# Performance work log

Hardware: AMD Instinct MI355X
Metric: run time of the kernel (lower is better)

The kernel has to match this reference:

```python
import jax, jax.numpy as jnp
import numpy as np

D_MODEL = 1024
N_HEADS = 16
HEAD = D_MODEL // N_HEADS
B, T = 4, 2048


def setup_inputs() -> dict:
    key = jax.random.key(0)
    ks = jax.random.split(key, 8)
    s = 0.02
    return {
        "x_enc": jax.random.normal(ks[0], (B, T, D_MODEL), dtype=jnp.float32),
        "x_dec": jax.random.normal(ks[1], (B, T, D_MODEL), dtype=jnp.float32),
        "mask": jnp.zeros((B, T, T), dtype=jnp.float32),
        "Wq": jax.random.normal(ks[2], (D_MODEL, D_MODEL), dtype=jnp.float32) * s,
        "bq": jnp.zeros((D_MODEL,), dtype=jnp.float32),
        "Wkv": jax.random.normal(ks[3], (D_MODEL, 2 * D_MODEL), dtype=jnp.float32) * s,
        "bkv": jnp.zeros((2 * D_MODEL,), dtype=jnp.float32),
        "Wo": jax.random.normal(ks[4], (D_MODEL, D_MODEL), dtype=jnp.float32) * s,
        "bo": jnp.zeros((D_MODEL,), dtype=jnp.float32),
    }


def reference(x_enc, x_dec, mask, Wq, bq, Wkv, bkv, Wo, bo):
    b, t, c = x_enc.shape
    # projections
    kv = x_enc @ Wkv + bkv                     # [B,T,2C]
    q = x_dec @ Wq + bq                        # [B,T,C]
    # split heads (replicates torch reshape of interleaved kv)
    kv = kv.reshape(b, t, N_HEADS, 2 * HEAD).transpose(0, 2, 1, 3)  # [B,H,T,2hs]
    q = q.reshape(b, t, N_HEADS, HEAD).transpose(0, 2, 1, 3)        # [B,H,T,hs]
    k, v = kv[..., :HEAD], kv[..., HEAD:]
    # attention
    scores = jnp.einsum("bhqd,bhkd->bhqk", q, k) / np.sqrt(HEAD).astype(np.float32)
    scores = scores + mask[:, None, :, :]      # additive mask, broadcast over heads
    attn = jax.nn.softmax(scores, axis=-1)
    res = jnp.einsum("bhqk,bhkd->bhqd", attn, v)   # [B,H,T,hs]
    res = res.transpose(0, 2, 1, 3).reshape(b, t, c)
    return res @ Wo + bo
```

## Files before the change

### kernel.cpp

```cpp
#include <hip/hip_runtime.h>
#include <hip/hip_bf16.h>
#include <math.h>


#define D_MODEL 1024
#define NH      16
#define HEAD    64
#define BATCH   4
#define SEQ     2048
#define QB      128

#define LOG2E   1.44269504088896f

typedef unsigned int   u32;
typedef unsigned short u16;
typedef __attribute__((ext_vector_type(8))) short s16x8;
typedef __attribute__((ext_vector_type(4))) float f32x4;

__device__ __forceinline__ u16 tobf(float f) {
    u32 u = __builtin_bit_cast(u32, f);
    return (u16)((u + 0x7fffu + ((u >> 16) & 1u)) >> 16);
}
__device__ __forceinline__ float frombf(u16 u) {
    return __builtin_bit_cast(float, (u32)u << 16);
}
__device__ __forceinline__ u32 cvtpk(float a, float b) {
    u32 r;
    asm("v_cvt_pk_bf16_f32 %0, %1, %2" : "=v"(r) : "v"(a), "v"(b));
    return r;
}

__device__ __forceinline__ void gl_lds16(const void* g, void* l) {
    __builtin_amdgcn_global_load_lds(
        (const __attribute__((address_space(1))) u32*)g,
        (__attribute__((address_space(3))) u32*)l, 16, 0, 0);
}

__global__ __launch_bounds__(256) void cast_bf16(
    const float* __restrict__ in, u16* __restrict__ out, int n)
{
    int i = (blockIdx.x * 256 + threadIdx.x) * 4;
    if (i < n) {
        float4 v = *(const float4*)(in + i);
        ushort4 o = make_ushort4(tobf(v.x), tobf(v.y), tobf(v.z), tobf(v.w));
        *(ushort4*)(out + i) = o;
    }
}

__global__ __launch_bounds__(256) void mask_prep(
    const float* __restrict__ mask, u16* __restrict__ mp)
{
    const size_t gt = (size_t)blockIdx.x * 256 + threadIdx.x;
    const int l = (int)(gt & 63);
    const size_t tile = gt >> 6;
    const int kt = (int)(tile & 127);
    const size_t bq = tile >> 7;
    const int qt = (int)(bq & 127);
    const int b  = (int)(bq >> 7);
    const int q15 = l & 15, quad = l >> 4;
    const int q = qt*16 + q15;
    const int k = kt*16 + quad*4;
    float4 v = *(const float4*)&mask[((size_t)(b*SEQ + q))*SEQ + k];
    ushort4 o = make_ushort4(tobf(v.x * LOG2E), tobf(v.y * LOG2E),
                             tobf(v.z * LOG2E), tobf(v.w * LOG2E));
    *(ushort4*)&mp[tile*256 + (size_t)l*4] = o;
}

__global__ __launch_bounds__(256) void transpose_cast(
    const float* __restrict__ W, u16* __restrict__ WT, int K, int N)
{
    __shared__ __align__(16) float tile[32][33];
    const int n0 = blockIdx.x * 32, k0 = blockIdx.y * 32;
    const int r = threadIdx.x >> 3, c4 = (threadIdx.x & 7) * 4;
    float4 v = *(const float4*)&W[(size_t)(k0 + r) * N + n0 + c4];
    tile[r][c4] = v.x; tile[r][c4+1] = v.y; tile[r][c4+2] = v.z; tile[r][c4+3] = v.w;
    __syncthreads();
    ushort4 o = make_ushort4(tobf(tile[c4+0][r]), tobf(tile[c4+1][r]),
                             tobf(tile[c4+2][r]), tobf(tile[c4+3][r]));
    *(ushort4*)&WT[(size_t)(n0 + r) * K + k0 + c4] = o;
}

__device__ __forceinline__ void store_out(u16* p, float v)  { *p = tobf(v); }
__device__ __forceinline__ void store_out(float* p, float v){ *p = v; }

template <typename OT>
__global__ __launch_bounds__(256) void gemm_bt(
    const u16* __restrict__ A, const u16* __restrict__ Bt,
    const float* __restrict__ bias, OT* __restrict__ C,
    int N, int K, float out_scale)
{
    __shared__ __align__(16) u16 As[128 * 32];
    __shared__ __align__(16) u16 Bs[128 * 32];
    const int t = threadIdx.x;
    const int w = t >> 6, l = t & 63;
    const int lane15 = l & 15, quad = l >> 4;
    const int m0 = blockIdx.y * 128, n0 = blockIdx.x * 128;
    const int wm = (w >> 1) * 64, wn = (w & 1) * 64;
    const int lr = l >> 2, lk = (l & 3) * 8;

    f32x4 acc[4][4] = {};

    for (int k0 = 0; k0 < K; k0 += 32) {
        __syncthreads();
        #pragma unroll
        for (int i = 0; i < 2; ++i) {
            const int chunk = w * 2 + i;
            gl_lds16(A  + (size_t)(m0 + chunk*16 + lr) * K + k0 + lk,
                     As + chunk * 512);
            gl_lds16(Bt + (size_t)(n0 + chunk*16 + lr) * K + k0 + lk,
                     Bs + chunk * 512);
        }
        __syncthreads();
        s16x8 af[4], bfr[4];
        #pragma unroll
        for (int i = 0; i < 4; ++i)
            af[i] = *(const s16x8*)&As[(wm + i*16 + lane15) * 32 + quad * 8];
        #pragma unroll
        for (int j = 0; j < 4; ++j)
            bfr[j] = *(const s16x8*)&Bs[(wn + j*16 + lane15) * 32 + quad * 8];
        #pragma unroll
        for (int i = 0; i < 4; ++i)
            #pragma unroll
            for (int j = 0; j < 4; ++j)
                acc[i][j] = __builtin_amdgcn_mfma_f32_16x16x32_bf16(
                    af[i], bfr[j], acc[i][j], 0, 0, 0);
    }
    #pragma unroll
    for (int j = 0; j < 4; ++j) {
        const int col = n0 + wn + j*16 + lane15;
        const float bv = bias[col];
        #pragma unroll
        for (int i = 0; i < 4; ++i)
            #pragma unroll
            for (int r = 0; r < 4; ++r) {
                const int row = m0 + wm + i*16 + quad*4 + r;
                store_out(C + (size_t)row * N + col, (acc[i][j][r] + bv) * out_scale);
            }
    }
}

__global__ __launch_bounds__(256) void v_transpose(
    const u16* __restrict__ kvb, u16* __restrict__ vt)
{
    __shared__ __align__(16) u16 tile[64][72];
    const int t  = threadIdx.x;
    const int t0 = blockIdx.x * 64;
    const int bh = blockIdx.y;
    const int b = bh >> 4, h = bh & 15;
    const int r = t >> 2, c = (t & 3) * 16;
    const u16* g = kvb + (size_t)(b*SEQ + t0 + r) * (2*D_MODEL) + h*128 + 64 + c;
    *(uint4*)&tile[r][c]     = *(const uint4*)g;
    *(uint4*)&tile[r][c + 8] = *(const uint4*)(g + 8);
    __syncthreads();
    u16 buf[16];
    #pragma unroll
    for (int i = 0; i < 16; ++i) buf[i] = tile[c + i][r];
    u16* o = vt + (size_t)(bh*64 + r) * SEQ + t0 + c;
    *(uint4*)o       = *(uint4*)&buf[0];
    *(uint4*)(o + 8) = *(uint4*)&buf[8];
}

__global__ __launch_bounds__(256, 3) void attn_mfma(
    const u16* __restrict__ qb, const u16* __restrict__ kvb,
    const u16* __restrict__ vt, const u16* __restrict__ mp,
    u16* __restrict__ resb)
{
    __shared__ __align__(16) u16 sm[4*4096 + 4*32*72];
    const int t = threadIdx.x;
    const int w = t >> 6, l = t & 63;
    const int lane15 = l & 15, quad = l >> 4;
    const int h  = blockIdx.x;
    const int q0 = blockIdx.y * QB;
    const int b  = blockIdx.z;
    const int bh = b * NH + h;
    const int lr4 = l >> 2;
    const int lc8 = (((l & 3) ^ (lr4 & 3)) * 8);
    const int cq  = (quad ^ (lane15 & 3)) * 8;

    s16x8 aq0[2], aq1[2];
    #pragma unroll
    for (int s = 0; s < 2; ++s) {
        const u16* qrow = qb + (size_t)(b*SEQ + q0 + w*32 + s*16 + lane15) * D_MODEL + h*HEAD;
        aq0[s] = *(const s16x8*)(qrow + quad*8);
        aq1[s] = *(const s16x8*)(qrow + 32 + quad*8);
    }
    const u16* mrow[2];
    #pragma unroll
    for (int s = 0; s < 2; ++s)
        mrow[s] = mp + (((size_t)b*128 + (q0>>4) + w*2 + s) * 128) * 256 + (size_t)l*4;

    auto stage = [&](int k0s, int bf) {
        #pragma unroll
        for (int i = 0; i < 2; ++i) {
            const int c = w*2 + i;
            const int hh = c & 1, rr = c >> 1;
            const u16* kg = kvb + (size_t)(b*SEQ + k0s + rr*16 + lr4) * (2*D_MODEL)
                                + h*128 + hh*32 + lc8;
            gl_lds16(kg, sm + bf*4096 + hh*2048 + rr*512);
            const u16* vg = vt + (size_t)(bh*64 + rr*16 + lr4) * SEQ
                               + k0s + hh*32 + lc8;
            gl_lds16(vg, sm + 8192 + bf*4096 + hh*2048 + rr*512);
        }
    };

    f32x4 o_acc[2][4] = {};
    f32x4 l_acc[2] = {};
    ushort4 mreg[2][4];
    s16x8 vones;
    #pragma unroll
    for (int i = 0; i < 8; ++i) vones[i] = (short)0x3F80;

    stage(0, 0);
    #pragma unroll
    for (int s = 0; s < 2; ++s)
        #pragma unroll
        for (int nt = 0; nt < 4; ++nt)
            mreg[s][nt] = *(const ushort4*)(mrow[s] + (size_t)nt * 256);

    u16* const Ps = sm + 16384;

    for (int it = 0; it < SEQ/64; ++it) {
        const int k0 = it * 64;
        const int bf = it & 1;
        __syncthreads();
        ushort4 mnxt[2][4];
        if (it + 1 < SEQ/64) {
            stage(k0 + 64, bf ^ 1);
            #pragma unroll
            for (int s = 0; s < 2; ++s)
                #pragma unroll
                for (int nt = 0; nt < 4; ++nt)
                    mnxt[s][nt] = *(const ushort4*)(mrow[s] + ((size_t)((k0+64)>>4) + nt) * 256);
        }

        s16x8 kf[4][2];
        #pragma unroll
        for (int nt = 0; nt < 4; ++nt) {
            kf[nt][0] = *(const s16x8*)(sm + bf*4096 +        (nt*16 + lane15)*32 + cq);
            kf[nt][1] = *(const s16x8*)(sm + bf*4096 + 2048 + (nt*16 + lane15)*32 + cq);
        }

        #pragma unroll
        for (int s = 0; s < 2; ++s) {
            f32x4 sv[4];
            #pragma unroll
            for (int nt = 0; nt < 4; ++nt) {
                sv[nt][0] = frombf(mreg[s][nt].x); sv[nt][1] = frombf(mreg[s][nt].y);
                sv[nt][2] = frombf(mreg[s][nt].z); sv[nt][3] = frombf(mreg[s][nt].w);
            }
            __builtin_amdgcn_s_setprio(1);
            #pragma unroll
            for (int nt = 0; nt < 4; ++nt) {
                sv[nt] = __builtin_amdgcn_mfma_f32_16x16x32_bf16(kf[nt][0], aq0[s], sv[nt], 0, 0, 0);
                sv[nt] = __builtin_amdgcn_mfma_f32_16x16x32_bf16(kf[nt][1], aq1[s], sv[nt], 0, 0, 0);
            }
            __builtin_amdgcn_s_setprio(0);
            u16* prow = Ps + (w*32 + s*16 + lane15) * 72;
            #pragma unroll
            for (int nt = 0; nt < 4; ++nt) {
                float p0 = exp2f(sv[nt][0]), p1 = exp2f(sv[nt][1]);
                float p2 = exp2f(sv[nt][2]), p3 = exp2f(sv[nt][3]);
                *(uint2*)&prow[nt*16 + quad*4] = make_uint2(cvtpk(p0, p1), cvtpk(p2, p3));
            }
        }

        s16x8 pf[2][2];
        #pragma unroll
        for (int s = 0; s < 2; ++s) {
            const u16* prow = Ps + (w*32 + s*16 + lane15) * 72;
            pf[s][0] = *(const s16x8*)&prow[quad*8];
            pf[s][1] = *(const s16x8*)&prow[32 + quad*8];
        }
        __builtin_amdgcn_s_setprio(1);
        #pragma unroll
        for (int s = 0; s < 2; ++s) {
            l_acc[s] = __builtin_amdgcn_mfma_f32_16x16x32_bf16(vones, pf[s][0], l_acc[s], 0, 0, 0);
            l_acc[s] = __builtin_amdgcn_mfma_f32_16x16x32_bf16(vones, pf[s][1], l_acc[s], 0, 0, 0);
        }
        #pragma unroll
        for (int dt = 0; dt < 4; ++dt) {
            s16x8 vf0 = *(const s16x8*)(sm + 8192 + bf*4096 +        (dt*16 + lane15)*32 + cq);
            s16x8 vf1 = *(const s16x8*)(sm + 8192 + bf*4096 + 2048 + (dt*16 + lane15)*32 + cq);
            #pragma unroll
            for (int s = 0; s < 2; ++s) {
                o_acc[s][dt] = __builtin_amdgcn_mfma_f32_16x16x32_bf16(vf0, pf[s][0], o_acc[s][dt], 0, 0, 0);
                o_acc[s][dt] = __builtin_amdgcn_mfma_f32_16x16x32_bf16(vf1, pf[s][1], o_acc[s][dt], 0, 0, 0);
            }
        }
        __builtin_amdgcn_s_setprio(0);

        if (it + 1 < SEQ/64) {
            #pragma unroll
            for (int s = 0; s < 2; ++s)
                #pragma unroll
                for (int nt = 0; nt < 4; ++nt)
                    mreg[s][nt] = mnxt[s][nt];
        }
    }

    __syncthreads();
    #pragma unroll
    for (int s = 0; s < 2; ++s) {
        const float inv = 1.f / l_acc[s][0];
        u16* orow = &sm[(w*32 + s*16 + lane15) * 72];
        #pragma unroll
        for (int dt = 0; dt < 4; ++dt) {
            *(uint2*)&orow[dt*16 + quad*4] = make_uint2(
                cvtpk(o_acc[s][dt][0]*inv, o_acc[s][dt][1]*inv),
                cvtpk(o_acc[s][dt][2]*inv, o_acc[s][dt][3]*inv));
        }
    }
    __syncthreads();
    {
        const int tr = t >> 1, tc = (t & 1) * 32;
        u16* o = resb + (size_t)(b*SEQ + q0 + tr) * D_MODEL + h*HEAD + tc;
        #pragma unroll
        for (int j = 0; j < 4; ++j)
            *(uint4*)(o + j*8) = *(const uint4*)&sm[tr*72 + tc + j*8];
    }
}

extern "C" void kernel_launch(void* const* d_in, const int* in_sizes, int n_in,
                              void* d_out, int out_size, void* d_ws, size_t ws_size,
                              hipStream_t stream) {
    const float* x_enc = (const float*)d_in[0];
    const float* x_dec = (const float*)d_in[1];
    const float* mask  = (const float*)d_in[2];
    const float* Wq    = (const float*)d_in[3];
    const float* bq    = (const float*)d_in[4];
    const float* Wkv   = (const float*)d_in[5];
    const float* bkv   = (const float*)d_in[6];
    const float* Wo    = (const float*)d_in[7];
    const float* bo    = (const float*)d_in[8];
    float* out = (float*)d_out;

    const int M = BATCH * SEQ;
    u16* xe   = (u16*)d_ws;
    u16* xd   = xe   + (size_t)M * D_MODEL;
    u16* wqT  = xd   + (size_t)M * D_MODEL;
    u16* wkvT = wqT  + (size_t)D_MODEL * D_MODEL;
    u16* woT  = wkvT + (size_t)2*D_MODEL*D_MODEL;
    u16* qbuf = woT  + (size_t)D_MODEL * D_MODEL;
    u16* kvb  = qbuf + (size_t)M * D_MODEL;
    u16* vtb  = kvb  + (size_t)M * 2 * D_MODEL;
    u16* resb = vtb  + (size_t)BATCH*NH*HEAD*SEQ;
    u16* mpk  = xe;

    const int NX = M * D_MODEL;
    cast_bf16<<<NX/1024, 256, 0, stream>>>(x_enc, xe, NX);
    cast_bf16<<<NX/1024, 256, 0, stream>>>(x_dec, xd, NX);
    transpose_cast<<<dim3(D_MODEL/32, D_MODEL/32), 256, 0, stream>>>(Wq,  wqT,  D_MODEL, D_MODEL);
    transpose_cast<<<dim3(2*D_MODEL/32, D_MODEL/32), 256, 0, stream>>>(Wkv, wkvT, D_MODEL, 2*D_MODEL);
    transpose_cast<<<dim3(D_MODEL/32, D_MODEL/32), 256, 0, stream>>>(Wo,  woT,  D_MODEL, D_MODEL);

    gemm_bt<u16><<<dim3(2*D_MODEL/128, M/128), 256, 0, stream>>>(
        xe, wkvT, bkv, kvb, 2*D_MODEL, D_MODEL, 1.0f);
    gemm_bt<u16><<<dim3(D_MODEL/128, M/128), 256, 0, stream>>>(
        xd, wqT, bq, qbuf, D_MODEL, D_MODEL, 0.125f * LOG2E);
    mask_prep<<<(BATCH*128*128*64)/256, 256, 0, stream>>>(mask, mpk);
    v_transpose<<<dim3(SEQ/64, BATCH*NH), 256, 0, stream>>>(kvb, vtb);
    attn_mfma<<<dim3(NH, SEQ/QB, BATCH), 256, 0, stream>>>(
        qbuf, kvb, vtb, mpk, resb);
    gemm_bt<float><<<dim3(D_MODEL/128, M/128), 256, 0, stream>>>(
        resb, woT, bo, out, D_MODEL, D_MODEL, 1.0f);
}
```

Baseline: 437.0 us.

## Keep softmax probabilities in registers by permuting K rows and mask layout

Reorders the K rows staged into LDS and the precomputed mask tile layout so that the S-tile MFMA output layout matches the B-operand layout the PV MFMA expects. Probabilities are exponentiated and packed straight into registers instead of being written to an LDS P buffer and read back. This removes that buffer, shrinking shared memory, and launch bounds rise to 4 blocks per CU. The risk is higher register pressure from holding all score tiles at once, which could cause spills under the tighter occupancy bound.

```diff
diff --git a/kernel.cpp b/kernel.cpp
--- a/kernel.cpp
+++ b/kernel.cpp
@@ -16,6 +16,7 @@
 typedef unsigned short u16;
 typedef __attribute__((ext_vector_type(8))) short s16x8;
 typedef __attribute__((ext_vector_type(4))) float f32x4;
+typedef __attribute__((ext_vector_type(4))) unsigned int u32v4;
 
 __device__ __forceinline__ u16 tobf(float f) {
     u32 u = __builtin_bit_cast(u32, f);
@@ -59,7 +60,7 @@
     const int b  = (int)(bq >> 7);
     const int q15 = l & 15, quad = l >> 4;
     const int q = qt*16 + q15;
-    const int k = kt*16 + quad*4;
+    const int k = (kt >> 2)*64 + ((kt >> 1) & 1)*32 + (kt & 1)*4 + quad*8;
     float4 v = *(const float4*)&mask[((size_t)(b*SEQ + q))*SEQ + k];
     ushort4 o = make_ushort4(tobf(v.x * LOG2E), tobf(v.y * LOG2E),
                              tobf(v.z * LOG2E), tobf(v.w * LOG2E));
@@ -160,12 +161,12 @@
     *(uint4*)(o + 8) = *(uint4*)&buf[8];
 }
 
-__global__ __launch_bounds__(256, 3) void attn_mfma(
+__global__ __launch_bounds__(256, 4) void attn_mfma(
     const u16* __restrict__ qb, const u16* __restrict__ kvb,
     const u16* __restrict__ vt, const u16* __restrict__ mp,
     u16* __restrict__ resb)
 {
-    __shared__ __align__(16) u16 sm[4*4096 + 4*32*72];
+    __shared__ __align__(16) u16 sm[4*4096];
     const int t = threadIdx.x;
     const int w = t >> 6, l = t & 63;
     const int lane15 = l & 15, quad = l >> 4;
@@ -176,6 +177,7 @@
     const int lr4 = l >> 2;
     const int lc8 = (((l & 3) ^ (lr4 & 3)) * 8);
     const int cq  = (quad ^ (lane15 & 3)) * 8;
+    const int kprow = (lr4 >> 2)*8 + (lr4 & 3);
 
     s16x8 aq0[2], aq1[2];
     #pragma unroll
@@ -194,7 +196,8 @@
         for (int i = 0; i < 2; ++i) {
             const int c = w*2 + i;
             const int hh = c & 1, rr = c >> 1;
-            const u16* kg = kvb + (size_t)(b*SEQ + k0s + rr*16 + lr4) * (2*D_MODEL)
+            const int krow = (rr >> 1)*32 + (rr & 1)*4 + kprow;
+            const u16* kg = kvb + (size_t)(b*SEQ + k0s + krow) * (2*D_MODEL)
                                 + h*128 + hh*32 + lc8;
             gl_lds16(kg, sm + bf*4096 + hh*2048 + rr*512);
             const u16* vg = vt + (size_t)(bh*64 + rr*16 + lr4) * SEQ
@@ -217,60 +220,55 @@
         for (int nt = 0; nt < 4; ++nt)
             mreg[s][nt] = *(const ushort4*)(mrow[s] + (size_t)nt * 256);
 
-    u16* const Ps = sm + 16384;
-
     for (int it = 0; it < SEQ/64; ++it) {
         const int k0 = it * 64;
         const int bf = it & 1;
         __syncthreads();
-        ushort4 mnxt[2][4];
+        if (it + 1 < SEQ/64)
+            stage(k0 + 64, bf ^ 1);
+
+        f32x4 sv[2][4];
+        #pragma unroll
+        for (int s = 0; s < 2; ++s)
+            #pragma unroll
+            for (int nt = 0; nt < 4; ++nt) {
+                sv[s][nt][0] = frombf(mreg[s][nt].x); sv[s][nt][1] = frombf(mreg[s][nt].y);
+                sv[s][nt][2] = frombf(mreg[s][nt].z); sv[s][nt][3] = frombf(mreg[s][nt].w);
+            }
+        __builtin_amdgcn_s_setprio(1);
+        #pragma unroll
+        for (int nt = 0; nt < 4; ++nt) {
+            s16x8 kf0 = *(const s16x8*)(sm + bf*4096 +        (nt*16 + lane15)*32 + cq);
+            s16x8 kf1 = *(const s16x8*)(sm + bf*4096 + 2048 + (nt*16 + lane15)*32 + cq);
+            #pragma unroll
+            for (int s = 0; s < 2; ++s) {
+                sv[s][nt] = __builtin_amdgcn_mfma_f32_16x16x32_bf16(kf0, aq0[s], sv[s][nt], 0, 0, 0);
+                sv[s][nt] = __builtin_amdgcn_mfma_f32_16x16x32_bf16(kf1, aq1[s], sv[s][nt], 0, 0, 0);
+            }
+        }
+        __builtin_amdgcn_s_setprio(0);
+
         if (it + 1 < SEQ/64) {
-            stage(k0 + 64, bf ^ 1);
             #pragma unroll
             for (int s = 0; s < 2; ++s)
                 #pragma unroll
                 for (int nt = 0; nt < 4; ++nt)
-                    mnxt[s][nt] = *(const ushort4*)(mrow[s] + ((size_t)((k0+64)>>4) + nt) * 256);
-        }
-
-        s16x8 kf[4][2];
-        #pragma unroll
-        for (int nt = 0; nt < 4; ++nt) {
-            kf[nt][0] = *(const s16x8*)(sm + bf*4096 +        (nt*16 + lane15)*32 + cq);
-            kf[nt][1] = *(const s16x8*)(sm + bf*4096 + 2048 + (nt*16 + lane15)*32 + cq);
-        }
-
-        #pragma unroll
-        for (int s = 0; s < 2; ++s) {
-            f32x4 sv[4];
-            #pragma unroll
-            for (int nt = 0; nt < 4; ++nt) {
-                sv[nt][0] = frombf(mreg[s][nt].x); sv[nt][1] = frombf(mreg[s][nt].y);
-                sv[nt][2] = frombf(mreg[s][nt].z); sv[nt][3] = frombf(mreg[s][nt].w);
-            }
-            __builtin_amdgcn_s_setprio(1);
-            #pragma unroll
-            for (int nt = 0; nt < 4; ++nt) {
-                sv[nt] = __builtin_amdgcn_mfma_f32_16x16x32_bf16(kf[nt][0], aq0[s], sv[nt], 0, 0, 0);
-                sv[nt] = __builtin_amdgcn_mfma_f32_16x16x32_bf16(kf[nt][1], aq1[s], sv[nt], 0, 0, 0);
-            }
-            __builtin_amdgcn_s_setprio(0);
-            u16* prow = Ps + (w*32 + s*16 + lane15) * 72;
-            #pragma unroll
-            for (int nt = 0; nt < 4; ++nt) {
-                float p0 = exp2f(sv[nt][0]), p1 = exp2f(sv[nt][1]);
-                float p2 = exp2f(sv[nt][2]), p3 = exp2f(sv[nt][3]);
-                *(uint2*)&prow[nt*16 + quad*4] = make_uint2(cvtpk(p0, p1), cvtpk(p2, p3));
-            }
+                    mreg[s][nt] = *(const ushort4*)(mrow[s] + ((size_t)((k0+64)>>4) + nt) * 256);
         }
 
         s16x8 pf[2][2];
         #pragma unroll
-        for (int s = 0; s < 2; ++s) {
-            const u16* prow = Ps + (w*32 + s*16 + lane15) * 72;
-            pf[s][0] = *(const s16x8*)&prow[quad*8];
-            pf[s][1] = *(const s16x8*)&prow[32 + quad*8];
-        }
+        for (int s = 0; s < 2; ++s)
+            #pragma unroll
+            for (int hf = 0; hf < 2; ++hf) {
+                u32v4 pk;
+                pk[0] = cvtpk(exp2f(sv[s][2*hf][0]),   exp2f(sv[s][2*hf][1]));
+                pk[1] = cvtpk(exp2f(sv[s][2*hf][2]),   exp2f(sv[s][2*hf][3]));
+                pk[2] = cvtpk(exp2f(sv[s][2*hf+1][0]), exp2f(sv[s][2*hf+1][1]));
+                pk[3] = cvtpk(exp2f(sv[s][2*hf+1][2]), exp2f(sv[s][2*hf+1][3]));
+                pf[s][hf] = __builtin_bit_cast(s16x8, pk);
+            }
+
         __builtin_amdgcn_s_setprio(1);
         #pragma unroll
         for (int s = 0; s < 2; ++s) {
@@ -288,14 +286,6 @@
             }
         }
         __builtin_amdgcn_s_setprio(0);
-
-        if (it + 1 < SEQ/64) {
-            #pragma unroll
-            for (int s = 0; s < 2; ++s)
-                #pragma unroll
-                for (int nt = 0; nt < 4; ++nt)
-                    mreg[s][nt] = mnxt[s][nt];
-        }
     }
 
     __syncthreads();
```

Result: faster. 427.7 us (-2.1%).
